# Kernel optimization log

Hardware: AMD Instinct MI355X
Metric: run time of the kernel (lower is better)

The kernel has to match this reference:

```python
import jax, jax.numpy as jnp
import numpy as np

B, H, W, C = 8, 64, 64, 256
CK = C // 8  # key/query dim of conv_f / conv_g


def setup_inputs() -> dict:
    key = jax.random.key(0)
    ks = jax.random.split(key, 10)
    s = lambda fan_in: 1.0 / np.sqrt(fan_in)
    return {
        "x": jax.random.normal(ks[0], (B, H, W, C), dtype=jnp.float32),
        "Wf": jax.random.normal(ks[1], (C, CK), dtype=jnp.float32) * s(C),
        "bf": jnp.zeros((CK,), dtype=jnp.float32),
        "Wg": jax.random.normal(ks[2], (C, CK), dtype=jnp.float32) * s(C),
        "bg": jnp.zeros((CK,), dtype=jnp.float32),
        "Wh": jax.random.normal(ks[3], (C, C), dtype=jnp.float32) * s(C),
        "bh": jnp.zeros((C,), dtype=jnp.float32),
        "Wo": jax.random.normal(ks[4], (C, C), dtype=jnp.float32) * s(C),
        "bo": jnp.zeros((C,), dtype=jnp.float32),
        # original init is zeros; use a random scalar so output/grads are nontrivial
        "gamma": jax.random.normal(ks[5], (1,), dtype=jnp.float32),
    }


def reference(x, Wf, bf, Wg, bg, Wh, bh, Wo, bo, gamma):
    b, h, w, c = x.shape
    n = h * w
    xf = x.reshape(b, n, c)                       # flatten spatial: [B, N, C]
    # 1x1 convs == per-pixel matmuls
    f = xf @ Wf + bf                              # [B, N, C//8]
    g = xf @ Wg + bg                              # [B, N, C//8]
    hh = xf @ Wh + bh                             # [B, N, C]
    # scores[b, i, j] = <g_i, f_j>; softmax over j (keys)
    scores = jnp.einsum("bnd,bmd->bnm", g, f)     # [B, N, N]
    attn = jax.nn.softmax(scores, axis=-1)
    o = jnp.einsum("bnm,bmc->bnc", attn, hh)      # [B, N, C]
    o = o @ Wo + bo                               # conv_o (1x1)
    out = gamma * o + xf                          # gamma residual
    return out.reshape(b, h, w, c)
```

## Files before the change

### kernel.cpp

```cpp
#include <hip/hip_runtime.h>
#include <hip/hip_fp16.h>
#include <hip/hip_bf16.h>

constexpr int BB  = 8;
constexpr int NN  = 4096;
constexpr int CC  = 256;
constexpr int CKK = 32;

typedef __attribute__((ext_vector_type(8))) short    short8;
typedef __attribute__((ext_vector_type(8))) _Float16 half8;
typedef __attribute__((ext_vector_type(4))) _Float16 half4;
typedef __attribute__((ext_vector_type(4))) float    f32x4;

__device__ __forceinline__ unsigned short bf16_bits(float v) {
    __hip_bfloat16 h = __float2bfloat16(v);
    return *reinterpret_cast<unsigned short*>(&h);
}
__device__ __forceinline__ float bf16_val(unsigned short u) {
    __hip_bfloat16 h = *reinterpret_cast<__hip_bfloat16*>(&u);
    return __bfloat162float(h);
}

__global__ __launch_bounds__(256) void prep_kernel(
    const float* __restrict__ Wf, const float* __restrict__ Wg,
    const float* __restrict__ Wh, const float* __restrict__ Wo,
    unsigned short* __restrict__ WThi, unsigned short* __restrict__ WTlo)
{
    const int n = blockIdx.x;
    const int k = threadIdx.x;
    float v;
    if      (n < 256) v = Wh[k * 256 + n];
    else if (n < 288) v = Wf[k * 32 + (n - 256)];
    else if (n < 320) v = Wg[k * 32 + (n - 288)];
    else              v = Wo[k * 256 + (n - 320)];
    const unsigned short hi = bf16_bits(v);
    WThi[n * 256 + k] = hi;
    WTlo[n * 256 + k] = bf16_bits(v - bf16_val(hi));
}

__global__ __launch_bounds__(256) void fgh_kernel(
    const float* __restrict__ x,
    const unsigned short* __restrict__ WThi, const unsigned short* __restrict__ WTlo,
    const float* __restrict__ bf, const float* __restrict__ bg,
    const float* __restrict__ bh,
    _Float16* __restrict__ fbuf, _Float16* __restrict__ gbuf,
    _Float16* __restrict__ hhT)
{
    const int tid = threadIdx.x, w = tid >> 6, lane = tid & 63;
    const int ln = lane & 15, lq = lane >> 4;
    const int px0 = blockIdx.x * 256 + w * 64;
    const int n0  = blockIdx.y * 64;

    f32x4 acc[4][4];
    #pragma unroll
    for (int i = 0; i < 4; ++i)
        #pragma unroll
        for (int j = 0; j < 4; ++j) acc[i][j] = {0.f, 0.f, 0.f, 0.f};

    #pragma unroll 1
    for (int kc = 0; kc < 8; ++kc) {
        const int k0 = kc * 32;
        short8 Ahi[4], Alo[4];
        #pragma unroll
        for (int mt = 0; mt < 4; ++mt) {
            float av[8];
            const float* xp = &x[(size_t)(px0 + mt * 16 + ln) * CC + k0 + lq * 8];
            *(float4*)&av[0] = *(const float4*)xp;
            *(float4*)&av[4] = *(const float4*)(xp + 4);
            #pragma unroll
            for (int j = 0; j < 8; ++j) {
                const unsigned short h = bf16_bits(av[j]);
                Ahi[mt][j] = (short)h;
                Alo[mt][j] = (short)bf16_bits(av[j] - bf16_val(h));
            }
        }
        #pragma unroll
        for (int nt = 0; nt < 4; ++nt) {
            const size_t boff = (size_t)(n0 + nt * 16 + ln) * 256 + k0 + lq * 8;
            const short8 Bhi = *(const short8*)&WThi[boff];
            const short8 Blo = *(const short8*)&WTlo[boff];
            #pragma unroll
            for (int mt = 0; mt < 4; ++mt) {
                acc[mt][nt] = __builtin_amdgcn_mfma_f32_16x16x32_bf16(Ahi[mt], Bhi, acc[mt][nt], 0, 0, 0);
                acc[mt][nt] = __builtin_amdgcn_mfma_f32_16x16x32_bf16(Ahi[mt], Blo, acc[mt][nt], 0, 0, 0);
                acc[mt][nt] = __builtin_amdgcn_mfma_f32_16x16x32_bf16(Alo[mt], Bhi, acc[mt][nt], 0, 0, 0);
            }
        }
    }

    const int b = px0 >> 12;
    if (blockIdx.y < 4) {
        #pragma unroll
        for (int nt = 0; nt < 4; ++nt) {
            const int c = n0 + nt * 16 + ln;
            const float bias = bh[c];
            #pragma unroll
            for (int mt = 0; mt < 4; ++mt) {
                half4 hv;
                #pragma unroll
                for (int r = 0; r < 4; ++r) hv[r] = (_Float16)(acc[mt][nt][r] + bias);
                const int npix = (px0 & (NN - 1)) + mt * 16 + lq * 4;
                *(half4*)&hhT[((size_t)(b * CC + c)) * NN + npix] = hv;
            }
        }
    } else {
        #pragma unroll
        for (int nt = 0; nt < 4; ++nt) {
            const int d = (nt & 1) * 16 + ln;
            const float bias = (nt < 2) ? bf[d] : bg[d];
            _Float16* dst = (nt < 2) ? fbuf : gbuf;
            #pragma unroll
            for (int mt = 0; mt < 4; ++mt)
                #pragma unroll
                for (int r = 0; r < 4; ++r)
                    dst[(size_t)(px0 + mt * 16 + lq * 4 + r) * CKK + d] =
                        (_Float16)(acc[mt][nt][r] + bias);
        }
    }
}

__global__ __launch_bounds__(256) void attn_kernel(
    const _Float16* __restrict__ fbuf, const _Float16* __restrict__ gbuf,
    const _Float16* __restrict__ hhT, float* __restrict__ obuf)
{
    __shared__ _Float16 P[2][64 * 72];
    __shared__ float mxbuf[4][64];
    __shared__ float rsbuf[4][64];

    const int tid = threadIdx.x, w = tid >> 6, lane = tid & 63;
    const int ln = lane & 15, lq = lane >> 4;
    const int b  = blockIdx.x & 7;
    const int q0 = (blockIdx.x >> 3) * 64;
    const int cb = w * 64;

    const f32x4 zero = {0.f, 0.f, 0.f, 0.f};
    constexpr float LOG2E = 1.4426950408889634f;

    half8 Bg[4];
    #pragma unroll
    for (int qt = 0; qt < 4; ++qt)
        Bg[qt] = *(const half8*)&gbuf[(size_t)(b * NN + q0 + qt * 16 + ln) * CKK + lq * 8];

    float mx[4];
    #pragma unroll
    for (int qt = 0; qt < 4; ++qt) mx[qt] = -1e30f;
    #pragma unroll 1
    for (int j0 = 0; j0 < NN; j0 += 64) {
        const half8 Af = *(const half8*)
            &fbuf[(size_t)(b * NN + j0 + w * 16 + ln) * CKK + lq * 8];
        #pragma unroll
        for (int qt = 0; qt < 4; ++qt) {
            const f32x4 s = __builtin_amdgcn_mfma_f32_16x16x32_f16(Af, Bg[qt], zero, 0, 0, 0);
            mx[qt] = fmaxf(mx[qt], fmaxf(fmaxf(s[0], s[1]), fmaxf(s[2], s[3])));
        }
    }
    #pragma unroll
    for (int qt = 0; qt < 4; ++qt) {
        mx[qt] = fmaxf(mx[qt], __shfl_xor(mx[qt], 16));
        mx[qt] = fmaxf(mx[qt], __shfl_xor(mx[qt], 32));
    }
    if (lane < 16) {
        #pragma unroll
        for (int qt = 0; qt < 4; ++qt) mxbuf[w][qt * 16 + ln] = mx[qt];
    }
    __syncthreads();
    float mk[4];
    #pragma unroll
    for (int qt = 0; qt < 4; ++qt)
        mk[qt] = LOG2E * fmaxf(fmaxf(mxbuf[0][qt * 16 + ln], mxbuf[1][qt * 16 + ln]),
                               fmaxf(mxbuf[2][qt * 16 + ln], mxbuf[3][qt * 16 + ln]));

    f32x4 O[4][4];
    #pragma unroll
    for (int qt = 0; qt < 4; ++qt)
        #pragma unroll
        for (int ct = 0; ct < 4; ++ct) O[qt][ct] = zero;
    float psum[4] = {0.f, 0.f, 0.f, 0.f};

    #pragma unroll 1
    for (int j0 = 0; j0 < NN; j0 += 64) {
        const int buf = (j0 >> 6) & 1;

        half8 Bh[4][2];
        #pragma unroll
        for (int ct = 0; ct < 4; ++ct)
            #pragma unroll
            for (int kh = 0; kh < 2; ++kh)
                Bh[ct][kh] = *(const half8*)
                    &hhT[((size_t)(b * CC + cb + ct * 16 + ln)) * NN + j0 + kh * 32 + lq * 8];

        const half8 Af = *(const half8*)
            &fbuf[(size_t)(b * NN + j0 + w * 16 + ln) * CKK + lq * 8];
        #pragma unroll
        for (int qt = 0; qt < 4; ++qt) {
            const f32x4 s = __builtin_amdgcn_mfma_f32_16x16x32_f16(Af, Bg[qt], zero, 0, 0, 0);
            half4 ph;
            float ps = 0.f;
            #pragma unroll
            for (int r = 0; r < 4; ++r) {
                const float p = exp2f(fmaf(s[r], LOG2E, -mk[qt]));
                ps += p;
                ph[r] = (_Float16)p;
            }
            psum[qt] += ps;
            *(half4*)&P[buf][(qt * 16 + ln) * 72 + w * 16 + lq * 4] = ph;
        }
        __syncthreads();

        #pragma unroll
        for (int qt = 0; qt < 4; ++qt) {
            const half8 Ap0 = *(const half8*)&P[buf][(qt * 16 + ln) * 72 + lq * 8];
            const half8 Ap1 = *(const half8*)&P[buf][(qt * 16 + ln) * 72 + 32 + lq * 8];
            #pragma unroll
            for (int ct = 0; ct < 4; ++ct) {
                O[qt][ct] = __builtin_amdgcn_mfma_f32_16x16x32_f16(Ap0, Bh[ct][0], O[qt][ct], 0, 0, 0);
                O[qt][ct] = __builtin_amdgcn_mfma_f32_16x16x32_f16(Ap1, Bh[ct][1], O[qt][ct], 0, 0, 0);
            }
        }
    }

    #pragma unroll
    for (int qt = 0; qt < 4; ++qt) {
        psum[qt] += __shfl_xor(psum[qt], 16);
        psum[qt] += __shfl_xor(psum[qt], 32);
    }
    if (lane < 16) {
        #pragma unroll
        for (int qt = 0; qt < 4; ++qt) rsbuf[w][qt * 16 + ln] = psum[qt];
    }
    __syncthreads();

    #pragma unroll
    for (int qt = 0; qt < 4; ++qt)
        #pragma unroll
        for (int r = 0; r < 4; ++r) {
            const int q = qt * 16 + lq * 4 + r;
            const float rinv = 1.0f / (rsbuf[0][q] + rsbuf[1][q] + rsbuf[2][q] + rsbuf[3][q]);
            #pragma unroll
            for (int ct = 0; ct < 4; ++ct)
                obuf[((size_t)(b * NN + q0 + q)) * CC + cb + ct * 16 + ln] = O[qt][ct][r] * rinv;
        }
}

__global__ __launch_bounds__(256) void out_kernel(
    const float* __restrict__ obuf,
    const unsigned short* __restrict__ WThi, const unsigned short* __restrict__ WTlo,
    const float* __restrict__ bo, const float* __restrict__ gamma,
    const float* __restrict__ x, float* __restrict__ out)
{
    const int tid = threadIdx.x, w = tid >> 6, lane = tid & 63;
    const int ln = lane & 15, lq = lane >> 4;
    const int px0 = blockIdx.x * 256 + w * 64;
    const int n0  = blockIdx.y * 64;

    f32x4 acc[4][4];
    #pragma unroll
    for (int i = 0; i < 4; ++i)
        #pragma unroll
        for (int j = 0; j < 4; ++j) acc[i][j] = {0.f, 0.f, 0.f, 0.f};

    #pragma unroll 1
    for (int kc = 0; kc < 8; ++kc) {
        const int k0 = kc * 32;
        short8 Ahi[4], Alo[4];
        #pragma unroll
        for (int mt = 0; mt < 4; ++mt) {
            float av[8];
            const float* op = &obuf[(size_t)(px0 + mt * 16 + ln) * CC + k0 + lq * 8];
            *(float4*)&av[0] = *(const float4*)op;
            *(float4*)&av[4] = *(const float4*)(op + 4);
            #pragma unroll
            for (int j = 0; j < 8; ++j) {
                const unsigned short h = bf16_bits(av[j]);
                Ahi[mt][j] = (short)h;
                Alo[mt][j] = (short)bf16_bits(av[j] - bf16_val(h));
            }
        }
        #pragma unroll
        for (int nt = 0; nt < 4; ++nt) {
            const size_t boff = (size_t)(320 + n0 + nt * 16 + ln) * 256 + k0 + lq * 8;
            const short8 Bhi = *(const short8*)&WThi[boff];
            const short8 Blo = *(const short8*)&WTlo[boff];
            #pragma unroll
            for (int mt = 0; mt < 4; ++mt) {
                acc[mt][nt] = __builtin_amdgcn_mfma_f32_16x16x32_bf16(Ahi[mt], Bhi, acc[mt][nt], 0, 0, 0);
                acc[mt][nt] = __builtin_amdgcn_mfma_f32_16x16x32_bf16(Ahi[mt], Blo, acc[mt][nt], 0, 0, 0);
                acc[mt][nt] = __builtin_amdgcn_mfma_f32_16x16x32_bf16(Alo[mt], Bhi, acc[mt][nt], 0, 0, 0);
            }
        }
    }

    const float gm = gamma[0];
    #pragma unroll
    for (int nt = 0; nt < 4; ++nt) {
        const int c = n0 + nt * 16 + ln;
        const float bias = bo[c];
        #pragma unroll
        for (int mt = 0; mt < 4; ++mt)
            #pragma unroll
            for (int r = 0; r < 4; ++r) {
                const size_t idx = (size_t)(px0 + mt * 16 + lq * 4 + r) * CC + c;
                out[idx] = gm * (acc[mt][nt][r] + bias) + x[idx];
            }
    }
}

extern "C" void kernel_launch(void* const* d_in, const int* in_sizes, int n_in,
                              void* d_out, int out_size, void* d_ws, size_t ws_size,
                              hipStream_t stream)
{
    (void)in_sizes; (void)n_in; (void)out_size; (void)ws_size;

    const float* x     = (const float*)d_in[0];
    const float* Wf    = (const float*)d_in[1];
    const float* bf    = (const float*)d_in[2];
    const float* Wg    = (const float*)d_in[3];
    const float* bg    = (const float*)d_in[4];
    const float* Wh    = (const float*)d_in[5];
    const float* bh    = (const float*)d_in[6];
    const float* Wo    = (const float*)d_in[7];
    const float* bo    = (const float*)d_in[8];
    const float* gamma = (const float*)d_in[9];
    float* out = (float*)d_out;

    _Float16* fbuf = (_Float16*)d_ws;
    _Float16* gbuf = fbuf + (size_t)BB * NN * CKK;
    _Float16* hhT  = gbuf + (size_t)BB * NN * CKK;
    float*    obuf = (float*)(hhT + (size_t)BB * CC * NN);
    unsigned short* WThi = (unsigned short*)(obuf + (size_t)BB * NN * CC);
    unsigned short* WTlo = WThi + (size_t)576 * 256;

    prep_kernel<<<576, 256, 0, stream>>>(Wf, Wg, Wh, Wo, WThi, WTlo);
    fgh_kernel<<<dim3(BB * NN / 256, 5), 256, 0, stream>>>(x, WThi, WTlo, bf, bg, bh,
                                                           fbuf, gbuf, hhT);
    attn_kernel<<<BB * NN / 64, 256, 0, stream>>>(fbuf, gbuf, hhT, obuf);
    out_kernel<<<dim3(BB * NN / 256, 4), 256, 0, stream>>>(obuf, WThi, WTlo, bo, gamma, x, out);
}
```

Baseline: 332.2 us.

## Restructure attention to stage swizzled H tiles in LDS with async loads

The attention kernel now gives each wave 16 queries across all 256 channels instead of 64 channels across 64 queries. H tiles are staged into double-buffered LDS with global_load_lds, and the softmax probabilities move between lanes by register shuffles instead of a shared P buffer. hhT is written with an XOR swizzle so LDS reads avoid bank conflicts, and the max pass prefetches the f tiles. The fp32 to bf16 hi/lo split is moved out of the GEMM loops into a separate xsplit kernel and the attention epilogue. This removes repeated conversion work but adds an extra pass over x and uses more workspace and registers.

After: 335.0 us. No clear change (+0.8%).

```diff
diff --git a/kernel.cpp b/kernel.cpp
--- a/kernel.cpp
+++ b/kernel.cpp
@@ -11,6 +11,9 @@
 typedef __attribute__((ext_vector_type(8))) _Float16 half8;
 typedef __attribute__((ext_vector_type(4))) _Float16 half4;
 typedef __attribute__((ext_vector_type(4))) float    f32x4;
+
+#define GPTR(x) ((const __attribute__((address_space(1))) void*)(x))
+#define LPTR(x) ((__attribute__((address_space(3))) void*)(x))
 
 __device__ __forceinline__ unsigned short bf16_bits(float v) {
     __hip_bfloat16 h = __float2bfloat16(v);
@@ -38,8 +41,27 @@
     WTlo[n * 256 + k] = bf16_bits(v - bf16_val(hi));
 }
 
+__global__ __launch_bounds__(256) void xsplit_kernel(
+    const float* __restrict__ x,
+    unsigned short* __restrict__ xhi, unsigned short* __restrict__ xlo)
+{
+    const size_t i = ((size_t)blockIdx.x * 256 + threadIdx.x) * 8;
+    float a[8];
+    *(float4*)&a[0] = *(const float4*)&x[i];
+    *(float4*)&a[4] = *(const float4*)&x[i + 4];
+    short8 hi, lo;
+    #pragma unroll
+    for (int j = 0; j < 8; ++j) {
+        const unsigned short h = bf16_bits(a[j]);
+        hi[j] = (short)h;
+        lo[j] = (short)bf16_bits(a[j] - bf16_val(h));
+    }
+    *(short8*)&xhi[i] = hi;
+    *(short8*)&xlo[i] = lo;
+}
+
 __global__ __launch_bounds__(256) void fgh_kernel(
-    const float* __restrict__ x,
+    const unsigned short* __restrict__ xhi, const unsigned short* __restrict__ xlo,
     const unsigned short* __restrict__ WThi, const unsigned short* __restrict__ WTlo,
     const float* __restrict__ bf, const float* __restrict__ bg,
     const float* __restrict__ bh,
@@ -63,16 +85,9 @@
         short8 Ahi[4], Alo[4];
         #pragma unroll
         for (int mt = 0; mt < 4; ++mt) {
-            float av[8];
-            const float* xp = &x[(size_t)(px0 + mt * 16 + ln) * CC + k0 + lq * 8];
-            *(float4*)&av[0] = *(const float4*)xp;
-            *(float4*)&av[4] = *(const float4*)(xp + 4);
-            #pragma unroll
-            for (int j = 0; j < 8; ++j) {
-                const unsigned short h = bf16_bits(av[j]);
-                Ahi[mt][j] = (short)h;
-                Alo[mt][j] = (short)bf16_bits(av[j] - bf16_val(h));
-            }
+            const size_t aoff = (size_t)(px0 + mt * 16 + ln) * CC + k0 + lq * 8;
+            Ahi[mt] = *(const short8*)&xhi[aoff];
+            Alo[mt] = *(const short8*)&xlo[aoff];
         }
         #pragma unroll
         for (int nt = 0; nt < 4; ++nt) {
@@ -100,7 +115,8 @@
                 #pragma unroll
                 for (int r = 0; r < 4; ++r) hv[r] = (_Float16)(acc[mt][nt][r] + bias);
                 const int npix = (px0 & (NN - 1)) + mt * 16 + lq * 4;
-                *(half4*)&hhT[((size_t)(b * CC + c)) * NN + npix] = hv;
+                const int nsw  = (npix & ~63) | (((((npix >> 3) & 7) ^ (ln & 7)) << 3) | (npix & 7));
+                *(half4*)&hhT[((size_t)(b * CC + c)) * NN + nsw] = hv;
             }
         }
     } else {
@@ -119,131 +135,158 @@
     }
 }
 
-__global__ __launch_bounds__(256) void attn_kernel(
+__global__ __launch_bounds__(256, 2) void attn_kernel(
     const _Float16* __restrict__ fbuf, const _Float16* __restrict__ gbuf,
-    const _Float16* __restrict__ hhT, float* __restrict__ obuf)
-{
-    __shared__ _Float16 P[2][64 * 72];
-    __shared__ float mxbuf[4][64];
-    __shared__ float rsbuf[4][64];
+    const _Float16* __restrict__ hhT,
+    unsigned short* __restrict__ ohi, unsigned short* __restrict__ olo)
+{
+    __shared__ _Float16 Ht[2][256 * 64];
 
     const int tid = threadIdx.x, w = tid >> 6, lane = tid & 63;
     const int ln = lane & 15, lq = lane >> 4;
     const int b  = blockIdx.x & 7;
     const int q0 = (blockIdx.x >> 3) * 64;
-    const int cb = w * 64;
+    const int qw = q0 + w * 16;
 
     const f32x4 zero = {0.f, 0.f, 0.f, 0.f};
     constexpr float LOG2E = 1.4426950408889634f;
-
-    half8 Bg[4];
-    #pragma unroll
-    for (int qt = 0; qt < 4; ++qt)
-        Bg[qt] = *(const half8*)&gbuf[(size_t)(b * NN + q0 + qt * 16 + ln) * CKK + lq * 8];
-
-    float mx[4];
-    #pragma unroll
-    for (int qt = 0; qt < 4; ++qt) mx[qt] = -1e30f;
+    const _Float16* fb = fbuf + (size_t)b * NN * CKK;
+
+    const _Float16* gsrc = hhT + ((size_t)(b * CC + w * 64 + (lane >> 3))) * NN + (lane & 7) * 8;
+
+    #pragma unroll
+    for (int i = 0; i < 8; ++i)
+        __builtin_amdgcn_global_load_lds(GPTR(gsrc + (size_t)i * 8 * NN),
+                                         LPTR(&Ht[0][(w * 64 + i * 8) * 64]), 16, 0, 0);
+
+    const half8 Bg = *(const half8*)&gbuf[(size_t)(b * NN + qw + ln) * CKK + lq * 8];
+
+    half8 Af[4], Afn[4];
+    #pragma unroll
+    for (int kt = 0; kt < 4; ++kt)
+        Af[kt] = *(const half8*)&fb[(size_t)(kt * 16 + ln) * CKK + lq * 8];
+    float mx = -1e30f;
     #pragma unroll 1
     for (int j0 = 0; j0 < NN; j0 += 64) {
-        const half8 Af = *(const half8*)
-            &fbuf[(size_t)(b * NN + j0 + w * 16 + ln) * CKK + lq * 8];
-        #pragma unroll
-        for (int qt = 0; qt < 4; ++qt) {
-            const f32x4 s = __builtin_amdgcn_mfma_f32_16x16x32_f16(Af, Bg[qt], zero, 0, 0, 0);
-            mx[qt] = fmaxf(mx[qt], fmaxf(fmaxf(s[0], s[1]), fmaxf(s[2], s[3])));
-        }
-    }
-    #pragma unroll
-    for (int qt = 0; qt < 4; ++qt) {
-        mx[qt] = fmaxf(mx[qt], __shfl_xor(mx[qt], 16));
-        mx[qt] = fmaxf(mx[qt], __shfl_xor(mx[qt], 32));
-    }
-    if (lane < 16) {
-        #pragma unroll
-        for (int qt = 0; qt < 4; ++qt) mxbuf[w][qt * 16 + ln] = mx[qt];
-    }
-    __syncthreads();
-    float mk[4];
-    #pragma unroll
-    for (int qt = 0; qt < 4; ++qt)
-        mk[qt] = LOG2E * fmaxf(fmaxf(mxbuf[0][qt * 16 + ln], mxbuf[1][qt * 16 + ln]),
-                               fmaxf(mxbuf[2][qt * 16 + ln], mxbuf[3][qt * 16 + ln]));
-
-    f32x4 O[4][4];
-    #pragma unroll
-    for (int qt = 0; qt < 4; ++qt)
-        #pragma unroll
-        for (int ct = 0; ct < 4; ++ct) O[qt][ct] = zero;
-    float psum[4] = {0.f, 0.f, 0.f, 0.f};
+        if (j0 + 64 < NN) {
+            #pragma unroll
+            for (int kt = 0; kt < 4; ++kt)
+                Afn[kt] = *(const half8*)&fb[(size_t)(j0 + 64 + kt * 16 + ln) * CKK + lq * 8];
+        }
+        #pragma unroll
+        for (int kt = 0; kt < 4; ++kt) {
+            const f32x4 s = __builtin_amdgcn_mfma_f32_16x16x32_f16(Af[kt], Bg, zero, 0, 0, 0);
+            mx = fmaxf(mx, fmaxf(fmaxf(s[0], s[1]), fmaxf(s[2], s[3])));
+        }
+        #pragma unroll
+        for (int kt = 0; kt < 4; ++kt) Af[kt] = Afn[kt];
+    }
+    mx = fmaxf(mx, __shfl_xor(mx, 16));
+    mx = fmaxf(mx, __shfl_xor(mx, 32));
+    const float mk = mx * LOG2E;
+
+    f32x4 O[16];
+    #pragma unroll
+    for (int ct = 0; ct < 16; ++ct) O[ct] = zero;
+    float psum = 0.f;
+
+    #pragma unroll
+    for (int kt = 0; kt < 4; ++kt)
+        Af[kt] = *(const half8*)&fb[(size_t)(kt * 16 + ln) * CKK + lq * 8];
+
+    const int s0lane = ln + (lq & 1) * 32;
+    const int s1lane = s0lane + 16;
+    const bool sel = (lq & 2) != 0;
 
     #pragma unroll 1
     for (int j0 = 0; j0 < NN; j0 += 64) {
         const int buf = (j0 >> 6) & 1;
 
-        half8 Bh[4][2];
-        #pragma unroll
-        for (int ct = 0; ct < 4; ++ct)
-            #pragma unroll
-            for (int kh = 0; kh < 2; ++kh)
-                Bh[ct][kh] = *(const half8*)
-                    &hhT[((size_t)(b * CC + cb + ct * 16 + ln)) * NN + j0 + kh * 32 + lq * 8];
-
-        const half8 Af = *(const half8*)
-            &fbuf[(size_t)(b * NN + j0 + w * 16 + ln) * CKK + lq * 8];
-        #pragma unroll
-        for (int qt = 0; qt < 4; ++qt) {
-            const f32x4 s = __builtin_amdgcn_mfma_f32_16x16x32_f16(Af, Bg[qt], zero, 0, 0, 0);
-            half4 ph;
-            float ps = 0.f;
+        __asm__ volatile("s_waitcnt vmcnt(0)" ::: "memory");
+        __syncthreads();
+
+        if (j0 + 64 < NN) {
+            const _Float16* gs = gsrc + j0 + 64;
+            #pragma unroll
+            for (int i = 0; i < 8; ++i)
+                __builtin_amdgcn_global_load_lds(GPTR(gs + (size_t)i * 8 * NN),
+                                                 LPTR(&Ht[buf ^ 1][(w * 64 + i * 8) * 64]), 16, 0, 0);
+            #pragma unroll
+            for (int kt = 0; kt < 4; ++kt)
+                Afn[kt] = *(const half8*)&fb[(size_t)(j0 + 64 + kt * 16 + ln) * CKK + lq * 8];
+        }
+
+        union H4 { half4 h; int2 i; } ph[4];
+        #pragma unroll
+        for (int kt = 0; kt < 4; ++kt) {
+            const f32x4 s = __builtin_amdgcn_mfma_f32_16x16x32_f16(Af[kt], Bg, zero, 0, 0, 0);
             #pragma unroll
             for (int r = 0; r < 4; ++r) {
-                const float p = exp2f(fmaf(s[r], LOG2E, -mk[qt]));
-                ps += p;
-                ph[r] = (_Float16)p;
-            }
-            psum[qt] += ps;
-            *(half4*)&P[buf][(qt * 16 + ln) * 72 + w * 16 + lq * 4] = ph;
-        }
-        __syncthreads();
-
-        #pragma unroll
-        for (int qt = 0; qt < 4; ++qt) {
-            const half8 Ap0 = *(const half8*)&P[buf][(qt * 16 + ln) * 72 + lq * 8];
-            const half8 Ap1 = *(const half8*)&P[buf][(qt * 16 + ln) * 72 + 32 + lq * 8];
-            #pragma unroll
-            for (int ct = 0; ct < 4; ++ct) {
-                O[qt][ct] = __builtin_amdgcn_mfma_f32_16x16x32_f16(Ap0, Bh[ct][0], O[qt][ct], 0, 0, 0);
-                O[qt][ct] = __builtin_amdgcn_mfma_f32_16x16x32_f16(Ap1, Bh[ct][1], O[qt][ct], 0, 0, 0);
-            }
-        }
-    }
-
-    #pragma unroll
-    for (int qt = 0; qt < 4; ++qt) {
-        psum[qt] += __shfl_xor(psum[qt], 16);
-        psum[qt] += __shfl_xor(psum[qt], 32);
-    }
-    if (lane < 16) {
-        #pragma unroll
-        for (int qt = 0; qt < 4; ++qt) rsbuf[w][qt * 16 + ln] = psum[qt];
-    }
-    __syncthreads();
-
-    #pragma unroll
-    for (int qt = 0; qt < 4; ++qt)
+                const float p = exp2f(fmaf(s[r], LOG2E, -mk));
+                psum += p;
+                ph[kt].h[r] = (_Float16)p;
+            }
+        }
+
+        union H8 { half8 h; int4 i; } apl, aph;
+        {
+            const int t0x0 = __shfl(ph[0].i.x, s0lane), t1x0 = __shfl(ph[1].i.x, s0lane);
+            const int t0y0 = __shfl(ph[0].i.y, s0lane), t1y0 = __shfl(ph[1].i.y, s0lane);
+            const int t0x1 = __shfl(ph[0].i.x, s1lane), t1x1 = __shfl(ph[1].i.x, s1lane);
+            const int t0y1 = __shfl(ph[0].i.y, s1lane), t1y1 = __shfl(ph[1].i.y, s1lane);
+            apl.i.x = sel ? t1x0 : t0x0;
+            apl.i.y = sel ? t1y0 : t0y0;
+            apl.i.z = sel ? t1x1 : t0x1;
+            apl.i.w = sel ? t1y1 : t0y1;
+        }
+        {
+            const int t2x0 = __shfl(ph[2].i.x, s0lane), t3x0 = __shfl(ph[3].i.x, s0lane);
+            const int t2y0 = __shfl(ph[2].i.y, s0lane), t3y0 = __shfl(ph[3].i.y, s0lane);
+            const int t2x1 = __shfl(ph[2].i.x, s1lane), t3x1 = __shfl(ph[3].i.x, s1lane);
+            const int t2y1 = __shfl(ph[2].i.y, s1lane), t3y1 = __shfl(ph[3].i.y, s1lane);
+            aph.i.x = sel ? t3x0 : t2x0;
+            aph.i.y = sel ? t3y0 : t2y0;
+            aph.i.z = sel ? t3x1 : t2x1;
+            aph.i.w = sel ? t3y1 : t2y1;
+        }
+
+        #pragma unroll
+        for (int ct = 0; ct < 16; ++ct) {
+            const int row = ct * 16 + ln;
+            const int sg0 = (lq ^ (ln & 7)) * 8;
+            const int sg1 = ((4 + lq) ^ (ln & 7)) * 8;
+            const half8 Bh0 = *(const half8*)&Ht[buf][row * 64 + sg0];
+            const half8 Bh1 = *(const half8*)&Ht[buf][row * 64 + sg1];
+            O[ct] = __builtin_amdgcn_mfma_f32_16x16x32_f16(apl.h, Bh0, O[ct], 0, 0, 0);
+            O[ct] = __builtin_amdgcn_mfma_f32_16x16x32_f16(aph.h, Bh1, O[ct], 0, 0, 0);
+        }
+
+        #pragma unroll
+        for (int kt = 0; kt < 4; ++kt) Af[kt] = Afn[kt];
+    }
+
+    psum += __shfl_xor(psum, 16);
+    psum += __shfl_xor(psum, 32);
+    float rinv[4];
+    #pragma unroll
+    for (int r = 0; r < 4; ++r) rinv[r] = 1.0f / __shfl(psum, lq * 4 + r);
+
+    #pragma unroll
+    for (int ct = 0; ct < 16; ++ct) {
+        const int c = ct * 16 + ln;
         #pragma unroll
         for (int r = 0; r < 4; ++r) {
-            const int q = qt * 16 + lq * 4 + r;
-            const float rinv = 1.0f / (rsbuf[0][q] + rsbuf[1][q] + rsbuf[2][q] + rsbuf[3][q]);
-            #pragma unroll
-            for (int ct = 0; ct < 4; ++ct)
-                obuf[((size_t)(b * NN + q0 + q)) * CC + cb + ct * 16 + ln] = O[qt][ct][r] * rinv;
-        }
+            const float v = O[ct][r] * rinv[r];
+            const unsigned short h = bf16_bits(v);
+            const size_t idx = (size_t)(b * NN + qw + lq * 4 + r) * CC + c;
+            ohi[idx] = h;
+            olo[idx] = bf16_bits(v - bf16_val(h));
+        }
+    }
 }
 
 __global__ __launch_bounds__(256) void out_kernel(
-    const float* __restrict__ obuf,
+    const unsigned short* __restrict__ ohi, const unsigned short* __restrict__ olo,
     const unsigned short* __restrict__ WThi, const unsigned short* __restrict__ WTlo,
     const float* __restrict__ bo, const float* __restrict__ gamma,
     const float* __restrict__ x, float* __restrict__ out)
@@ -265,16 +308,9 @@
         short8 Ahi[4], Alo[4];
         #pragma unroll
         for (int mt = 0; mt < 4; ++mt) {
-            float av[8];
-            const float* op = &obuf[(size_t)(px0 + mt * 16 + ln) * CC + k0 + lq * 8];
-            *(float4*)&av[0] = *(const float4*)op;
-            *(float4*)&av[4] = *(const float4*)(op + 4);
-            #pragma unroll
-            for (int j = 0; j < 8; ++j) {
-                const unsigned short h = bf16_bits(av[j]);
-                Ahi[mt][j] = (short)h;
-                Alo[mt][j] = (short)bf16_bits(av[j] - bf16_val(h));
-            }
+            const size_t aoff = (size_t)(px0 + mt * 16 + ln) * CC + k0 + lq * 8;
+            Ahi[mt] = *(const short8*)&ohi[aoff];
+            Alo[mt] = *(const short8*)&olo[aoff];
         }
         #pragma unroll
         for (int nt = 0; nt < 4; ++nt) {
@@ -326,13 +362,16 @@
     _Float16* fbuf = (_Float16*)d_ws;
     _Float16* gbuf = fbuf + (size_t)BB * NN * CKK;
     _Float16* hhT  = gbuf + (size_t)BB * NN * CKK;
-    float*    obuf = (float*)(hhT + (size_t)BB * CC * NN);
-    unsigned short* WThi = (unsigned short*)(obuf + (size_t)BB * NN * CC);
+    unsigned short* r1 = (unsigned short*)(hhT + (size_t)BB * CC * NN);
+    unsigned short* r2 = r1 + (size_t)BB * NN * CC;
+    unsigned short* WThi = r2 + (size_t)BB * NN * CC;
     unsigned short* WTlo = WThi + (size_t)576 * 256;
 
+    xsplit_kernel<<<BB * NN * CC / (256 * 8), 256, 0, stream>>>(x, r1, r2);
     prep_kernel<<<576, 256, 0, stream>>>(Wf, Wg, Wh, Wo, WThi, WTlo);
-    fgh_kernel<<<dim3(BB * NN / 256, 5), 256, 0, stream>>>(x, WThi, WTlo, bf, bg, bh,
-                                                           fbuf, gbuf, hhT);
-    attn_kernel<<<BB * NN / 64, 256, 0, stream>>>(fbuf, gbuf, hhT, obuf);
-    out_kernel<<<dim3(BB * NN / 256, 4), 256, 0, stream>>>(obuf, WThi, WTlo, bo, gamma, x, out);
-}
+    fgh_kernel<<<dim3(BB * NN / 256, 5), 256, 0, stream>>>(r1, r2, WThi, WTlo,
+                                                           bf, bg, bh, fbuf, gbuf, hhT);
+    attn_kernel<<<BB * NN / 64, 256, 0, stream>>>(fbuf, gbuf, hhT, r1, r2);
+    out_kernel<<<dim3(BB * NN / 256, 4), 256, 0, stream>>>(r1, r2, WThi, WTlo,
+                                                           bo, gamma, x, out);
+}
```
